# Kernel optimization log

Hardware: AMD Instinct MI355X
Metric: run time of the kernel (lower is better)

## Reference

```python
import jax, jax.numpy as jnp
import numpy as np

N_NODES = 100000
N_GRAPHS = 64
NEG_SLOPE = 0.1


def lrelu(x):
    return jnp.where(x > 0, x, NEG_SLOPE * x)


def gcn_layer(x, W, b, src, dst, deg_inv_sqrt):
    # PyG GCNConv: x' = D^-1/2 (A + I) D^-1/2 (x W) + b
    h = x @ W  # [N, out]
    norm = (deg_inv_sqrt[src] * deg_inv_sqrt[dst])[:, None]  # [E, 1]
    agg = jax.ops.segment_sum(h[src] * norm, dst, num_segments=N_NODES)
    agg = agg + h * (deg_inv_sqrt ** 2)[:, None]  # self-loop contribution
    return agg + b


def setup_inputs() -> dict:
    key = jax.random.key(0)
    ks = jax.random.split(key, 12)
    E = 1600000
    x = jax.random.normal(ks[0], (N_NODES, 128), dtype=jnp.float32)
    edge_index = jax.random.randint(ks[1], (2, E), 0, N_NODES, dtype=jnp.int32)
    batch = jnp.sort(jax.random.randint(ks[2], (N_NODES,), 0, N_GRAPHS, dtype=jnp.int32))

    def glorot(k, shape):
        fan_in, fan_out = shape
        s = jnp.sqrt(6.0 / (fan_in + fan_out))
        return jax.random.uniform(k, shape, jnp.float32, -s, s)

    return {
        "x": x,
        "edge_index": edge_index,
        "batch": batch,
        "W1": glorot(ks[3], (128, 32)),
        "b1": jnp.zeros((32,), jnp.float32),
        "W2": glorot(ks[4], (32, 64)),
        "b2": jnp.zeros((64,), jnp.float32),
        "Wl1": glorot(ks[5], (64, 128)),
        "bl1": jnp.zeros((128,), jnp.float32),
        "Wl2": glorot(ks[6], (128, 64)),
        "bl2": jnp.zeros((64,), jnp.float32),
        "Wl3": glorot(ks[7], (64, 1)),
        "bl3": jnp.zeros((1,), jnp.float32),
    }


def reference(x, edge_index, batch, W1, b1, W2, b2, Wl1, bl1, Wl2, bl2, Wl3, bl3):
    src, dst = edge_index[0], edge_index[1]
    # degree with self-loops (symmetric norm, all edge weights = 1)
    deg = jax.ops.segment_sum(jnp.ones_like(src, dtype=x.dtype), dst, num_segments=N_NODES) + 1.0
    deg_inv_sqrt = jax.lax.rsqrt(deg)

    h = lrelu(gcn_layer(x, W1, b1, src, dst, deg_inv_sqrt))
    h = gcn_layer(h, W2, b2, src, dst, deg_inv_sqrt)
    g = jax.ops.segment_max(h, batch, num_segments=N_GRAPHS)  # global max pool [G, 64]
    g = lrelu(g @ Wl1 + bl1)
    g = lrelu(g @ Wl2 + bl2)
    return g @ Wl3 + bl3  # [G, 1]
```

## Files before the change

kernel.cpp:

```cpp
#include <hip/hip_runtime.h>
#include <hip/hip_fp16.h>
#include <math.h>

#define N_NODES 100000
#define N_EDGES 1600000
#define N_GRAPHS 64
#define NB 391
#define CAP 5504

__device__ __forceinline__ unsigned f2o(float f) {
    unsigned u = __float_as_uint(f);
    return (u & 0x80000000u) ? ~u : (u | 0x80000000u);
}
__device__ __forceinline__ float o2f(unsigned u) {
    return (u & 0x80000000u) ? __uint_as_float(u & 0x7fffffffu) : __uint_as_float(~u);
}

__device__ __forceinline__ float4 cvt8(float2 raw) {
    __half2 h0 = ((const __half2*)&raw)[0];
    __half2 h1 = ((const __half2*)&raw)[1];
    float2 f0 = __half22float2(h0);
    float2 f1 = __half22float2(h1);
    return make_float4(f0.x, f0.y, f1.x, f1.y);
}
__device__ __forceinline__ float4 loadh8(const __half* p) {
    return cvt8(*(const float2*)p);
}
__device__ __forceinline__ void storeh8(__half* p, float4 v) {
    __half2 o0 = __floats2half2_rn(v.x, v.y);
    __half2 o1 = __floats2half2_rn(v.z, v.w);
    float2 ow;
    ((__half2*)&ow)[0] = o0;
    ((__half2*)&ow)[1] = o1;
    *(float2*)p = ow;
}

typedef _Float16 h2r __attribute__((ext_vector_type(2)));
typedef _Float16 h4  __attribute__((ext_vector_type(4)));
union HB { float4 f4; h2r h[4]; };
union H4 { float2 f2; h4 h; };

__global__ __launch_bounds__(256) void bucket_kernel(const int* __restrict__ src, const int* __restrict__ dst,
                                                     int* __restrict__ bucketCursor, unsigned* __restrict__ ebuf) {
    __shared__ int hist[NB];
    __shared__ int lbase[NB];
    __shared__ int lcur[NB];
    __shared__ int gbase[NB];
    __shared__ unsigned lbuf[3200];
    __shared__ unsigned short bkt[3200];
    int tid = threadIdx.x;
    for (int b = tid; b < NB; b += 256) hist[b] = 0;
    __syncthreads();
    int e0 = blockIdx.x * 3200;
    for (int i = tid; i < 3200; i += 256) {
        int d = dst[e0 + i];
        atomicAdd(&hist[d >> 8], 1);
    }
    __syncthreads();
    if (tid < 64) {
        int carry = 0;
        #pragma unroll
        for (int c = 0; c < 7; c++) {
            int idx = c * 64 + tid;
            int v = (idx < NB) ? hist[idx] : 0;
            int inc = v;
            #pragma unroll
            for (int o = 1; o < 64; o <<= 1) {
                int t = __shfl_up(inc, o, 64);
                if (tid >= o) inc += t;
            }
            if (idx < NB) lbase[idx] = carry + inc - v;
            carry += __shfl(inc, 63, 64);
        }
    }
    __syncthreads();
    for (int b = tid; b < NB; b += 256) {
        int h = hist[b];
        gbase[b] = h ? atomicAdd(&bucketCursor[b], h) : 0;
        lcur[b] = lbase[b];
    }
    __syncthreads();
    for (int i = tid; i < 3200; i += 256) {
        int d = dst[e0 + i];
        int s = src[e0 + i];
        int bu = d >> 8;
        int lp = atomicAdd(&lcur[bu], 1);
        lbuf[lp] = ((unsigned)(d & 255) << 24) | (unsigned)s;
        bkt[lp] = (unsigned short)bu;
    }
    __syncthreads();
    for (int i = tid; i < 3200; i += 256) {
        int bu = bkt[i];
        int off = gbase[bu] + (i - lbase[bu]);
        if (off < CAP)
            ebuf[(size_t)bu * CAP + off] = lbuf[i];
    }
}

__global__ __launch_bounds__(256) void csr_kernel(const unsigned* __restrict__ ebuf,
                                                  const int* __restrict__ bucketCursor,
                                                  int* __restrict__ colb, int* __restrict__ rowptr,
                                                  int* __restrict__ cnt, float* __restrict__ dis) {
    __shared__ unsigned stage1[CAP];
    __shared__ unsigned stage2[CAP];
    __shared__ int c256[256], row256[256], cur256[256];
    int b = blockIdx.x;
    int tid = threadIdx.x;
    int M = bucketCursor[b];
    if (M > CAP) M = CAP;
    c256[tid] = 0;
    __syncthreads();
    const unsigned* eb = ebuf + (size_t)b * CAP;
    for (int i = tid; i < M; i += 256) {
        unsigned v = eb[i];
        stage1[i] = v;
        atomicAdd(&c256[v >> 24], 1);
    }
    __syncthreads();
    if (tid < 64) {
        int c0 = c256[tid * 4], c1 = c256[tid * 4 + 1], c2 = c256[tid * 4 + 2], c3 = c256[tid * 4 + 3];
        int s = c0 + c1 + c2 + c3;
        int inc = s;
        #pragma unroll
        for (int o = 1; o < 64; o <<= 1) {
            int v = __shfl_up(inc, o, 64);
            if (tid >= o) inc += v;
        }
        int ex = inc - s;
        row256[tid * 4] = ex;
        row256[tid * 4 + 1] = ex + c0;
        row256[tid * 4 + 2] = ex + c0 + c1;
        row256[tid * 4 + 3] = ex + c0 + c1 + c2;
    }
    __syncthreads();
    cur256[tid] = row256[tid];
    int node = (b << 8) + tid;
    if (node < N_NODES) {
        int c = c256[tid];
        cnt[node] = c;
        dis[node] = rsqrtf((float)(c + 1));
        rowptr[node] = b * CAP + row256[tid];
    }
    __syncthreads();
    for (int i = tid; i < M; i += 256) {
        unsigned p = stage1[i];
        int slot = atomicAdd(&cur256[p >> 24], 1);
        stage2[slot] = p & 0xFFFFFFu;
    }
    __syncthreads();
    for (int i = tid; i < M; i += 256) colb[b * CAP + i] = (int)stage2[i];
}

__global__ __launch_bounds__(256) void gemm1_kernel(const float* __restrict__ x, const float* __restrict__ W1,
                                                    const float* __restrict__ dis, __half* __restrict__ hs1h) {
    __shared__ __half xsh[128][136];
    __shared__ __half wth[32][136];
    int tid = threadIdx.x;
    int r0 = blockIdx.x * 128;
    for (int idx = tid; idx < 128 * 32; idx += 256) {
        int k = idx >> 5, j = idx & 31;
        wth[j][k] = __float2half_rn(W1[idx]);
    }
    for (int idx = tid; idx < 128 * 32; idx += 256) {
        int r = idx >> 5, c4 = idx & 31;
        int gr = r0 + r;
        float4 v = (gr < N_NODES) ? ((const float4*)x)[(size_t)gr * 32 + c4] : make_float4(0.f, 0.f, 0.f, 0.f);
        __half* p = &xsh[r][c4 * 4];
        *(__half2*)p       = __floats2half2_rn(v.x, v.y);
        *(__half2*)(p + 2) = __floats2half2_rn(v.z, v.w);
    }
    __syncthreads();
    int jg = tid & 7;
    int rg = tid >> 3;
    float acc[4][4];
    #pragma unroll
    for (int i = 0; i < 4; i++)
        #pragma unroll
        for (int j = 0; j < 4; j++) acc[i][j] = 0.f;
    for (int kc = 0; kc < 128; kc += 8) {
        HB xr[4], wr[4];
        #pragma unroll
        for (int ri = 0; ri < 4; ri++) xr[ri].f4 = *(const float4*)&xsh[rg + 32 * ri][kc];
        #pragma unroll
        for (int jj = 0; jj < 4; jj++) wr[jj].f4 = *(const float4*)&wth[jg * 4 + jj][kc];
        #pragma unroll
        for (int ri = 0; ri < 4; ri++) {
            #pragma unroll
            for (int jj = 0; jj < 4; jj++) {
                #pragma unroll
                for (int t = 0; t < 4; t++) {
#if defined(__has_builtin) && __has_builtin(__builtin_amdgcn_fdot2)
                    acc[ri][jj] = __builtin_amdgcn_fdot2(xr[ri].h[t], wr[jj].h[t], acc[ri][jj], false);
#else
                    acc[ri][jj] += (float)xr[ri].h[t][0] * (float)wr[jj].h[t][0]
                                 + (float)xr[ri].h[t][1] * (float)wr[jj].h[t][1];
#endif
                }
            }
        }
    }
    #pragma unroll
    for (int ri = 0; ri < 4; ri++) {
        int gr = r0 + rg + 32 * ri;
        if (gr < N_NODES) {
            float dr = dis[gr];
            float2 ow;
            ((__half2*)&ow)[0] = __floats2half2_rn(dr * acc[ri][0], dr * acc[ri][1]);
            ((__half2*)&ow)[1] = __floats2half2_rn(dr * acc[ri][2], dr * acc[ri][3]);
            *(float2*)&hs1h[(size_t)gr * 32 + jg * 4] = ow;
        }
    }
}

__global__ __launch_bounds__(256) void agg1_kernel(const __half* __restrict__ hs1h, const int* __restrict__ colb,
                                                   const int* __restrict__ rowptr, const int* __restrict__ cnt,
                                                   const float* __restrict__ dis, const float* __restrict__ b1,
                                                   __half* __restrict__ t1h) {
    int tid = threadIdx.x;
    int wid = tid >> 6;
    int lane = tid & 63;
    int half = lane >> 5;
    int es = (lane >> 3) & 3;
    int q = lane & 7;
    int w = blockIdx.x * 4 + wid;
    int r0 = w * 4;

    H4 z; z.f2 = make_float2(0.f, 0.f);
    int r = r0 + half;
    int st = rowptr[r];
    int n = cnt[r];
    H4 pS = z, p0 = z, p1 = z, p2 = z, p3 = z, p4 = z, p5 = z;
    if (es == 0) pS.f2 = *(const float2*)(hs1h + (size_t)r * 32 + q * 4);
    {
        int e0 = es, e1 = 4 + es, e2 = 8 + es, e3 = 12 + es, e4 = 16 + es, e5 = 20 + es;
        if (e0 < n) p0.f2 = *(const float2*)(hs1h + (size_t)colb[st + e0] * 32 + q * 4);
        if (e1 < n) p1.f2 = *(const float2*)(hs1h + (size_t)colb[st + e1] * 32 + q * 4);
        if (e2 < n) p2.f2 = *(const float2*)(hs1h + (size_t)colb[st + e2] * 32 + q * 4);
        if (e3 < n) p3.f2 = *(const float2*)(hs1h + (size_t)colb[st + e3] * 32 + q * 4);
        if (e4 < n) p4.f2 = *(const float2*)(hs1h + (size_t)colb[st + e4] * 32 + q * 4);
        if (e5 < n) p5.f2 = *(const float2*)(hs1h + (size_t)colb[st + e5] * 32 + q * 4);
    }
    #pragma unroll
    for (int i = 0; i < 2; i++) {
        int rA = r;
        int stA = st, nA = n;
        H4 rS = pS, v0 = p0, v1 = p1, v2 = p2, v3 = p3, v4 = p4, v5 = p5;
        pS = z; p0 = z; p1 = z; p2 = z; p3 = z; p4 = z; p5 = z;
        if (i == 0) {
            r = r0 + 2 + half;
            st = rowptr[r];
            n = cnt[r];
            if (es == 0) pS.f2 = *(const float2*)(hs1h + (size_t)r * 32 + q * 4);
            int e0 = es, e1 = 4 + es, e2 = 8 + es, e3 = 12 + es, e4 = 16 + es, e5 = 20 + es;
            if (e0 < n) p0.f2 = *(const float2*)(hs1h + (size_t)colb[st + e0] * 32 + q * 4);
            if (e1 < n) p1.f2 = *(const float2*)(hs1h + (size_t)colb[st + e1] * 32 + q * 4);
            if (e2 < n) p2.f2 = *(const float2*)(hs1h + (size_t)colb[st + e2] * 32 + q * 4);
            if (e3 < n) p3.f2 = *(const float2*)(hs1h + (size_t)colb[st + e3] * 32 + q * 4);
            if (e4 < n) p4.f2 = *(const float2*)(hs1h + (size_t)colb[st + e4] * 32 + q * 4);
            if (e5 < n) p5.f2 = *(const float2*)(hs1h + (size_t)colb[st + e5] * 32 + q * 4);
        }
        h4 sh = (rS.h + (v0.h + v1.h)) + ((v2.h + v3.h) + (v4.h + v5.h));
        float4 a = make_float4((float)sh.x, (float)sh.y, (float)sh.z, (float)sh.w);
        for (int k = 24; k < nA; k += 8) {
            int e0 = k + es, e1 = k + 4 + es;
            if (e0 < nA) {
                float4 v = loadh8(hs1h + (size_t)colb[stA + e0] * 32 + q * 4);
                a.x += v.x; a.y += v.y; a.z += v.z; a.w += v.w;
            }
            if (e1 < nA) {
                float4 v = loadh8(hs1h + (size_t)colb[stA + e1] * 32 + q * 4);
                a.x += v.x; a.y += v.y; a.z += v.z; a.w += v.w;
            }
        }
        #pragma unroll
        for (int m = 8; m <= 16; m <<= 1) {
            a.x += __shfl_xor(a.x, m, 64);
            a.y += __shfl_xor(a.y, m, 64);
            a.z += __shfl_xor(a.z, m, 64);
            a.w += __shfl_xor(a.w, m, 64);
        }
        if (es == 0) {
            float4 bv = *(const float4*)&b1[q * 4];
            float dr = dis[rA];
            float4 v;
            v.x = dr * a.x + bv.x; v.y = dr * a.y + bv.y; v.z = dr * a.z + bv.z; v.w = dr * a.w + bv.w;
            v.x = v.x > 0.f ? v.x : 0.1f * v.x;
            v.y = v.y > 0.f ? v.y : 0.1f * v.y;
            v.z = v.z > 0.f ? v.z : 0.1f * v.z;
            v.w = v.w > 0.f ? v.w : 0.1f * v.w;
            v.x *= dr; v.y *= dr; v.z *= dr; v.w *= dr;
            storeh8(t1h + (size_t)rA * 32 + q * 4, v);
        }
    }
}

__global__ __launch_bounds__(1024) void agg2gemm_kernel(const __half* __restrict__ t1h, const int* __restrict__ colb,
                                                        const int* __restrict__ rowptr, const int* __restrict__ cnt,
                                                        const float* __restrict__ dis,
                                                        const float* __restrict__ W2, const float* __restrict__ b2,
                                                        const int* __restrict__ batch, unsigned* __restrict__ gbufu) {
    __shared__ float as1[64][32];
    __shared__ float w2s[32][64];
    __shared__ float red[16][64];
    int tid = threadIdx.x;
    int r0 = blockIdx.x * 64;
    for (int idx = tid; idx < 32 * 64; idx += 1024) w2s[idx >> 6][idx & 63] = W2[idx];

    int wid = tid >> 6;
    int lane = tid & 63;
    int half = lane >> 5;
    int es = (lane >> 3) & 3;
    int q = lane & 7;
    int base = r0 + wid * 4;

    H4 z; z.f2 = make_float2(0.f, 0.f);
    int r = base + half;
    bool vld = r < N_NODES;
    int st = vld ? rowptr[r] : 0;
    int n  = vld ? cnt[r] : 0;
    H4 pS = z, p0 = z, p1 = z, p2 = z, p3 = z, p4 = z, p5 = z;
    if (vld && es == 0) pS.f2 = *(const float2*)(t1h + (size_t)r * 32 + q * 4);
    {
        int e0 = es, e1 = 4 + es, e2 = 8 + es, e3 = 12 + es, e4 = 16 + es, e5 = 20 + es;
        if (e0 < n) p0.f2 = *(const float2*)(t1h + (size_t)colb[st + e0] * 32 + q * 4);
        if (e1 < n) p1.f2 = *(const float2*)(t1h + (size_t)colb[st + e1] * 32 + q * 4);
        if (e2 < n) p2.f2 = *(const float2*)(t1h + (size_t)colb[st + e2] * 32 + q * 4);
        if (e3 < n) p3.f2 = *(const float2*)(t1h + (size_t)colb[st + e3] * 32 + q * 4);
        if (e4 < n) p4.f2 = *(const float2*)(t1h + (size_t)colb[st + e4] * 32 + q * 4);
        if (e5 < n) p5.f2 = *(const float2*)(t1h + (size_t)colb[st + e5] * 32 + q * 4);
    }
    #pragma unroll
    for (int i = 0; i < 2; i++) {
        int rA = i * 2;
        int rAg = base + rA + half;
        bool vA = rAg < N_NODES;
        int stA = st, nA = n;
        H4 rS = pS, v0 = p0, v1 = p1, v2 = p2, v3 = p3, v4 = p4, v5 = p5;
        pS = z; p0 = z; p1 = z; p2 = z; p3 = z; p4 = z; p5 = z;
        if (i == 0) {
            r = base + 2 + half;
            vld = r < N_NODES;
            st = vld ? rowptr[r] : 0;
            n  = vld ? cnt[r] : 0;
            if (vld && es == 0) pS.f2 = *(const float2*)(t1h + (size_t)r * 32 + q * 4);
            int e0 = es, e1 = 4 + es, e2 = 8 + es, e3 = 12 + es, e4 = 16 + es, e5 = 20 + es;
            if (e0 < n) p0.f2 = *(const float2*)(t1h + (size_t)colb[st + e0] * 32 + q * 4);
            if (e1 < n) p1.f2 = *(const float2*)(t1h + (size_t)colb[st + e1] * 32 + q * 4);
            if (e2 < n) p2.f2 = *(const float2*)(t1h + (size_t)colb[st + e2] * 32 + q * 4);
            if (e3 < n) p3.f2 = *(const float2*)(t1h + (size_t)colb[st + e3] * 32 + q * 4);
            if (e4 < n) p4.f2 = *(const float2*)(t1h + (size_t)colb[st + e4] * 32 + q * 4);
            if (e5 < n) p5.f2 = *(const float2*)(t1h + (size_t)colb[st + e5] * 32 + q * 4);
        }
        h4 sh = (rS.h + (v0.h + v1.h)) + ((v2.h + v3.h) + (v4.h + v5.h));
        float4 a = make_float4((float)sh.x, (float)sh.y, (float)sh.z, (float)sh.w);
        for (int k = 24; k < nA; k += 8) {
            int e0 = k + es, e1 = k + 4 + es;
            if (e0 < nA) {
                float4 v = loadh8(t1h + (size_t)colb[stA + e0] * 32 + q * 4);
                a.x += v.x; a.y += v.y; a.z += v.z; a.w += v.w;
            }
            if (e1 < nA) {
                float4 v = loadh8(t1h + (size_t)colb[stA + e1] * 32 + q * 4);
                a.x += v.x; a.y += v.y; a.z += v.z; a.w += v.w;
            }
        }
        #pragma unroll
        for (int m = 8; m <= 16; m <<= 1) {
            a.x += __shfl_xor(a.x, m, 64);
            a.y += __shfl_xor(a.y, m, 64);
            a.z += __shfl_xor(a.z, m, 64);
            a.w += __shfl_xor(a.w, m, 64);
        }
        if (es == 0 && vA) {
            float dr = dis[rAg];
            float4 o = make_float4(dr * a.x, dr * a.y, dr * a.z, dr * a.w);
            *(float4*)&as1[wid * 4 + rA + half][q * 4] = o;
        }
    }
    __syncthreads();

    int j = tid & 63;
    int rq = tid >> 6;
    float w2c[32];
    #pragma unroll
    for (int k = 0; k < 32; k++) w2c[k] = w2s[k][j];
    float bj = b2[j];
    int rend = (r0 + 64 <= N_NODES) ? 64 : (N_NODES - r0);
    int gfirst = batch[r0];
    int glast = batch[r0 + rend - 1];
    bool uni = (gfirst == glast);
    float runmax = -INFINITY;
    #pragma unroll
    for (int i = 0; i < 4; i++) {
        int rl = rq + i * 16;
        if (rl >= rend) break;
        float acc = bj;
        #pragma unroll
        for (int kc = 0; kc < 32; kc += 4) {
            float4 av = *(const float4*)&as1[rl][kc];
            acc += av.x * w2c[kc] + av.y * w2c[kc + 1] + av.z * w2c[kc + 2] + av.w * w2c[kc + 3];
        }
        if (uni) runmax = fmaxf(runmax, acc);
        else atomicMax(&gbufu[batch[r0 + rl] * 64 + j], f2o(acc));
    }
    if (uni) {
        red[rq][j] = runmax;
        __syncthreads();
        if (tid < 64) {
            float m = -INFINITY;
            #pragma unroll
            for (int k = 0; k < 16; k++) m = fmaxf(m, red[k][tid]);
            atomicMax(&gbufu[gfirst * 64 + tid], f2o(m));
        }
    }
}

__global__ __launch_bounds__(256) void mlp_kernel(const unsigned* __restrict__ gbufu,
                                                  const float* __restrict__ Wl1, const float* __restrict__ bl1,
                                                  const float* __restrict__ Wl2, const float* __restrict__ bl2,
                                                  const float* __restrict__ Wl3, const float* __restrict__ bl3,
                                                  float* __restrict__ out) {
    __shared__ float A[64][64];
    __shared__ float B[64][128];
    int tid = threadIdx.x;
    for (int idx = tid; idx < 64 * 64; idx += 256) A[idx >> 6][idx & 63] = o2f(gbufu[idx]);
    __syncthreads();
    {
        int j = tid & 127;
        int rg = tid >> 7;
        float wc[64];
        #pragma unroll
        for (int k = 0; k < 64; k++) wc[k] = Wl1[k * 128 + j];
        float bj = bl1[j];
        for (int r = rg; r < 64; r += 2) {
            float acc = bj;
            #pragma unroll
            for (int kc = 0; kc < 64; kc += 4) {
                float4 av = *(const float4*)&A[r][kc];
                acc += av.x * wc[kc] + av.y * wc[kc + 1] + av.z * wc[kc + 2] + av.w * wc[kc + 3];
            }
            B[r][j] = acc > 0.f ? acc : 0.1f * acc;
        }
    }
    __syncthreads();
    {
        int j = tid & 63;
        int rg = tid >> 6;
        float wc[128];
        #pragma unroll
        for (int k = 0; k < 128; k++) wc[k] = Wl2[k * 64 + j];
        float bj = bl2[j];
        for (int r = rg; r < 64; r += 4) {
            float acc = bj;
            #pragma unroll
            for (int kc = 0; kc < 128; kc += 4) {
                float4 bv = *(const float4*)&B[r][kc];
                acc += bv.x * wc[kc] + bv.y * wc[kc + 1] + bv.z * wc[kc + 2] + bv.w * wc[kc + 3];
            }
            A[r][j] = acc > 0.f ? acc : 0.1f * acc;
        }
    }
    __syncthreads();
    if (tid < 64) {
        int r = tid;
        float acc = bl3[0];
        #pragma unroll
        for (int k = 0; k < 64; k++) acc += A[r][k] * Wl3[k];
        out[r] = acc;
    }
}

extern "C" void kernel_launch(void* const* d_in, const int* in_sizes, int n_in,
                              void* d_out, int out_size, void* d_ws, size_t ws_size,
                              hipStream_t stream) {
    (void)in_sizes; (void)n_in; (void)out_size; (void)ws_size;
    const float* x    = (const float*)d_in[0];
    const int*   edge = (const int*)d_in[1];
    const int*   batch= (const int*)d_in[2];
    const float* W1   = (const float*)d_in[3];
    const float* b1   = (const float*)d_in[4];
    const float* W2   = (const float*)d_in[5];
    const float* b2   = (const float*)d_in[6];
    const float* Wl1  = (const float*)d_in[7];
    const float* bl1  = (const float*)d_in[8];
    const float* Wl2  = (const float*)d_in[9];
    const float* bl2  = (const float*)d_in[10];
    const float* Wl3  = (const float*)d_in[11];
    const float* bl3  = (const float*)d_in[12];
    const int* srcp = edge;
    const int* dstp = edge + N_EDGES;

    char* ws = (char*)d_ws;
    int*      bucketCursor = (int*)ws;
    unsigned* gbufu        = (unsigned*)(bucketCursor + NB);
    size_t zeroed = (size_t)(NB + N_GRAPHS * 64) * 4;
    size_t off = (zeroed + 255) & ~(size_t)255;
    auto alloc = [&](size_t bytes) { char* p = ws + off; off = (off + bytes + 255) & ~(size_t)255; return p; };
    float*    dis    = (float*)alloc((size_t)N_NODES * 4);
    int*      cnt    = (int*)alloc((size_t)N_NODES * 4);
    int*      rowptr = (int*)alloc((size_t)N_NODES * 4);
    unsigned* ebuf   = (unsigned*)alloc((size_t)NB * CAP * 4);
    int*      colb   = (int*)alloc((size_t)NB * CAP * 4);
    __half*   hs1h   = (__half*)alloc((size_t)N_NODES * 32 * 2);
    __half*   t1h    = (__half*)alloc((size_t)N_NODES * 32 * 2);

    hipMemsetAsync(ws, 0, zeroed, stream);

    bucket_kernel  <<<500, 256, 0, stream>>>(srcp, dstp, bucketCursor, ebuf);
    csr_kernel     <<<NB, 256, 0, stream>>>(ebuf, bucketCursor, colb, rowptr, cnt, dis);
    gemm1_kernel   <<<(N_NODES + 127) / 128, 256, 0, stream>>>(x, W1, dis, hs1h);
    agg1_kernel    <<<6250, 256, 0, stream>>>(hs1h, colb, rowptr, cnt, dis, b1, t1h);
    agg2gemm_kernel<<<(N_NODES + 63) / 64, 1024, 0, stream>>>(t1h, colb, rowptr, cnt, dis, W2, b2, batch, gbufu);
    mlp_kernel     <<<1, 256, 0, stream>>>(gbufu, Wl1, bl1, Wl2, bl2, Wl3, bl3, (float*)d_out);
}
```

Before: 262.4 us.

## Replace CSR build with bucketed edge lists and LDS atomic aggregation

The full CSR construction (per-bucket sort into colb, rowptr, cnt) is dropped; the CSR kernel now only counts degrees to produce dis. Both aggregation kernels instead read the raw bucketed edge buffer. Each block takes one quarter of a 256-node bucket, compacts its edges into LDS with a ballot, gathers the source features and accumulates them with shared-memory float atomics. This removes the second sort pass and the colb/rowptr traffic. In exchange every block rescans the whole bucket, pays for LDS atomic contention, and silently drops edges beyond ELMAX=2048 per quarter.

```diff
diff --git a/kernel.cpp b/kernel.cpp
--- a/kernel.cpp
+++ b/kernel.cpp
@@ -7,6 +7,7 @@
 #define N_GRAPHS 64
 #define NB 391
 #define CAP 5504
+#define ELMAX 2048
 
 __device__ __forceinline__ unsigned f2o(float f) {
     unsigned u = __float_as_uint(f);
@@ -97,13 +98,10 @@
     }
 }
 
-__global__ __launch_bounds__(256) void csr_kernel(const unsigned* __restrict__ ebuf,
-                                                  const int* __restrict__ bucketCursor,
-                                                  int* __restrict__ colb, int* __restrict__ rowptr,
-                                                  int* __restrict__ cnt, float* __restrict__ dis) {
-    __shared__ unsigned stage1[CAP];
-    __shared__ unsigned stage2[CAP];
-    __shared__ int c256[256], row256[256], cur256[256];
+__global__ __launch_bounds__(256) void csrlite_kernel(const unsigned* __restrict__ ebuf,
+                                                      const int* __restrict__ bucketCursor,
+                                                      float* __restrict__ dis) {
+    __shared__ int c256[256];
     int b = blockIdx.x;
     int tid = threadIdx.x;
     int M = bucketCursor[b];
@@ -111,44 +109,10 @@
     c256[tid] = 0;
     __syncthreads();
     const unsigned* eb = ebuf + (size_t)b * CAP;
-    for (int i = tid; i < M; i += 256) {
-        unsigned v = eb[i];
-        stage1[i] = v;
-        atomicAdd(&c256[v >> 24], 1);
-    }
-    __syncthreads();
-    if (tid < 64) {
-        int c0 = c256[tid * 4], c1 = c256[tid * 4 + 1], c2 = c256[tid * 4 + 2], c3 = c256[tid * 4 + 3];
-        int s = c0 + c1 + c2 + c3;
-        int inc = s;
-        #pragma unroll
-        for (int o = 1; o < 64; o <<= 1) {
-            int v = __shfl_up(inc, o, 64);
-            if (tid >= o) inc += v;
-        }
-        int ex = inc - s;
-        row256[tid * 4] = ex;
-        row256[tid * 4 + 1] = ex + c0;
-        row256[tid * 4 + 2] = ex + c0 + c1;
-        row256[tid * 4 + 3] = ex + c0 + c1 + c2;
-    }
-    __syncthreads();
-    cur256[tid] = row256[tid];
+    for (int i = tid; i < M; i += 256) atomicAdd(&c256[eb[i] >> 24], 1);
+    __syncthreads();
     int node = (b << 8) + tid;
-    if (node < N_NODES) {
-        int c = c256[tid];
-        cnt[node] = c;
-        dis[node] = rsqrtf((float)(c + 1));
-        rowptr[node] = b * CAP + row256[tid];
-    }
-    __syncthreads();
-    for (int i = tid; i < M; i += 256) {
-        unsigned p = stage1[i];
-        int slot = atomicAdd(&cur256[p >> 24], 1);
-        stage2[slot] = p & 0xFFFFFFu;
-    }
-    __syncthreads();
-    for (int i = tid; i < M; i += 256) colb[b * CAP + i] = (int)stage2[i];
+    if (node < N_NODES) dis[node] = rsqrtf((float)(c256[tid] + 1));
 }
 
 __global__ __launch_bounds__(256) void gemm1_kernel(const float* __restrict__ x, const float* __restrict__ W1,
@@ -212,169 +176,194 @@
     }
 }
 
-__global__ __launch_bounds__(256) void agg1_kernel(const __half* __restrict__ hs1h, const int* __restrict__ colb,
-                                                   const int* __restrict__ rowptr, const int* __restrict__ cnt,
-                                                   const float* __restrict__ dis, const float* __restrict__ b1,
-                                                   __half* __restrict__ t1h) {
+#define ACCP 36
+
+__global__ __launch_bounds__(512) void agg1e_kernel(const __half* __restrict__ hs1h,
+                                                    const unsigned* __restrict__ ebuf,
+                                                    const int* __restrict__ bucketCursor,
+                                                    const float* __restrict__ dis, const float* __restrict__ b1,
+                                                    __half* __restrict__ t1h) {
+    __shared__ float acc[64][ACCP];
+    __shared__ unsigned elist[ELMAX];
+    __shared__ int ecnt;
     int tid = threadIdx.x;
+    int b = blockIdx.x >> 2;
+    int qt = blockIdx.x & 3;
+    int nb = (b << 8) + (qt << 6);
+    for (int i = tid; i < 64 * ACCP; i += 512) ((float*)acc)[i] = 0.f;
+    if (tid == 0) ecnt = 0;
+    __syncthreads();
+
+    int M = bucketCursor[b];
+    if (M > CAP) M = CAP;
+    const unsigned* eb = ebuf + (size_t)b * CAP;
+    int lane = tid & 63;
+    for (int i0 = 0; i0 < M; i0 += 512) {
+        int i = i0 + tid;
+        unsigned w = 0;
+        bool keep = false;
+        if (i < M) {
+            w = eb[i];
+            keep = ((w >> 30) == (unsigned)qt);
+        }
+        unsigned long long m = __ballot(keep);
+        int cnt = __popcll(m);
+        int base = 0;
+        if (lane == 0 && cnt) base = atomicAdd(&ecnt, cnt);
+        base = __shfl(base, 0, 64);
+        if (keep) {
+            int slot = base + __popcll(m & ((1ull << lane) - 1ull));
+            if (slot < ELMAX) elist[slot] = w;
+        }
+    }
+    __syncthreads();
+    int E = ecnt;
+    if (E > ELMAX) E = ELMAX;
+
     int wid = tid >> 6;
-    int lane = tid & 63;
-    int half = lane >> 5;
-    int es = (lane >> 3) & 3;
+    int e = lane >> 3;
     int q = lane & 7;
-    int w = blockIdx.x * 4 + wid;
-    int r0 = w * 4;
-
     H4 z; z.f2 = make_float2(0.f, 0.f);
-    int r = r0 + half;
-    int st = rowptr[r];
-    int n = cnt[r];
-    H4 pS = z, p0 = z, p1 = z, p2 = z, p3 = z, p4 = z, p5 = z;
-    if (es == 0) pS.f2 = *(const float2*)(hs1h + (size_t)r * 32 + q * 4);
+    H4 pv = z; int pdl = -1;
     {
-        int e0 = es, e1 = 4 + es, e2 = 8 + es, e3 = 12 + es, e4 = 16 + es, e5 = 20 + es;
-        if (e0 < n) p0.f2 = *(const float2*)(hs1h + (size_t)colb[st + e0] * 32 + q * 4);
-        if (e1 < n) p1.f2 = *(const float2*)(hs1h + (size_t)colb[st + e1] * 32 + q * 4);
-        if (e2 < n) p2.f2 = *(const float2*)(hs1h + (size_t)colb[st + e2] * 32 + q * 4);
-        if (e3 < n) p3.f2 = *(const float2*)(hs1h + (size_t)colb[st + e3] * 32 + q * 4);
-        if (e4 < n) p4.f2 = *(const float2*)(hs1h + (size_t)colb[st + e4] * 32 + q * 4);
-        if (e5 < n) p5.f2 = *(const float2*)(hs1h + (size_t)colb[st + e5] * 32 + q * 4);
-    }
-    #pragma unroll
-    for (int i = 0; i < 2; i++) {
-        int rA = r;
-        int stA = st, nA = n;
-        H4 rS = pS, v0 = p0, v1 = p1, v2 = p2, v3 = p3, v4 = p4, v5 = p5;
-        pS = z; p0 = z; p1 = z; p2 = z; p3 = z; p4 = z; p5 = z;
-        if (i == 0) {
-            r = r0 + 2 + half;
-            st = rowptr[r];
-            n = cnt[r];
-            if (es == 0) pS.f2 = *(const float2*)(hs1h + (size_t)r * 32 + q * 4);
-            int e0 = es, e1 = 4 + es, e2 = 8 + es, e3 = 12 + es, e4 = 16 + es, e5 = 20 + es;
-            if (e0 < n) p0.f2 = *(const float2*)(hs1h + (size_t)colb[st + e0] * 32 + q * 4);
-            if (e1 < n) p1.f2 = *(const float2*)(hs1h + (size_t)colb[st + e1] * 32 + q * 4);
-            if (e2 < n) p2.f2 = *(const float2*)(hs1h + (size_t)colb[st + e2] * 32 + q * 4);
-            if (e3 < n) p3.f2 = *(const float2*)(hs1h + (size_t)colb[st + e3] * 32 + q * 4);
-            if (e4 < n) p4.f2 = *(const float2*)(hs1h + (size_t)colb[st + e4] * 32 + q * 4);
-            if (e5 < n) p5.f2 = *(const float2*)(hs1h + (size_t)colb[st + e5] * 32 + q * 4);
-        }
-        h4 sh = (rS.h + (v0.h + v1.h)) + ((v2.h + v3.h) + (v4.h + v5.h));
-        float4 a = make_float4((float)sh.x, (float)sh.y, (float)sh.z, (float)sh.w);
-        for (int k = 24; k < nA; k += 8) {
-            int e0 = k + es, e1 = k + 4 + es;
-            if (e0 < nA) {
-                float4 v = loadh8(hs1h + (size_t)colb[stA + e0] * 32 + q * 4);
-                a.x += v.x; a.y += v.y; a.z += v.z; a.w += v.w;
-            }
-            if (e1 < nA) {
-                float4 v = loadh8(hs1h + (size_t)colb[stA + e1] * 32 + q * 4);
-                a.x += v.x; a.y += v.y; a.z += v.z; a.w += v.w;
-            }
-        }
-        #pragma unroll
-        for (int m = 8; m <= 16; m <<= 1) {
-            a.x += __shfl_xor(a.x, m, 64);
-            a.y += __shfl_xor(a.y, m, 64);
-            a.z += __shfl_xor(a.z, m, 64);
-            a.w += __shfl_xor(a.w, m, 64);
-        }
-        if (es == 0) {
-            float4 bv = *(const float4*)&b1[q * 4];
-            float dr = dis[rA];
-            float4 v;
-            v.x = dr * a.x + bv.x; v.y = dr * a.y + bv.y; v.z = dr * a.z + bv.z; v.w = dr * a.w + bv.w;
-            v.x = v.x > 0.f ? v.x : 0.1f * v.x;
-            v.y = v.y > 0.f ? v.y : 0.1f * v.y;
-            v.z = v.z > 0.f ? v.z : 0.1f * v.z;
-            v.w = v.w > 0.f ? v.w : 0.1f * v.w;
-            v.x *= dr; v.y *= dr; v.z *= dr; v.w *= dr;
-            storeh8(t1h + (size_t)rA * 32 + q * 4, v);
-        }
-    }
-}
-
-__global__ __launch_bounds__(1024) void agg2gemm_kernel(const __half* __restrict__ t1h, const int* __restrict__ colb,
-                                                        const int* __restrict__ rowptr, const int* __restrict__ cnt,
-                                                        const float* __restrict__ dis,
-                                                        const float* __restrict__ W2, const float* __restrict__ b2,
-                                                        const int* __restrict__ batch, unsigned* __restrict__ gbufu) {
-    __shared__ float as1[64][32];
+        int gi = wid * 8 + e;
+        if (gi < E) {
+            unsigned w = elist[gi];
+            pdl = (int)((w >> 24) & 63u);
+            pv.f2 = *(const float2*)(hs1h + (size_t)(w & 0xFFFFFFu) * 32 + q * 4);
+        }
+    }
+    for (int bi = wid * 8; bi < E; bi += 64) {
+        H4 cv = pv; int cdl = pdl;
+        pv = z; pdl = -1;
+        int gi = bi + 64 + e;
+        if (gi < E) {
+            unsigned w = elist[gi];
+            pdl = (int)((w >> 24) & 63u);
+            pv.f2 = *(const float2*)(hs1h + (size_t)(w & 0xFFFFFFu) * 32 + q * 4);
+        }
+        if (cdl >= 0) {
+            float4 f = cvt8(cv.f2);
+            atomicAdd(&acc[cdl][q * 4 + 0], f.x);
+            atomicAdd(&acc[cdl][q * 4 + 1], f.y);
+            atomicAdd(&acc[cdl][q * 4 + 2], f.z);
+            atomicAdd(&acc[cdl][q * 4 + 3], f.w);
+        }
+    }
+    __syncthreads();
+
+    int row = tid >> 3, qc = tid & 7;
+    int node = nb + row;
+    if (node < N_NODES) {
+        float dr = dis[node];
+        float4 s = loadh8(hs1h + (size_t)node * 32 + qc * 4);
+        float4 a = *(const float4*)&acc[row][qc * 4];
+        float4 bv = *(const float4*)&b1[qc * 4];
+        float4 v;
+        v.x = dr * (a.x + s.x) + bv.x;
+        v.y = dr * (a.y + s.y) + bv.y;
+        v.z = dr * (a.z + s.z) + bv.z;
+        v.w = dr * (a.w + s.w) + bv.w;
+        v.x = v.x > 0.f ? v.x : 0.1f * v.x;
+        v.y = v.y > 0.f ? v.y : 0.1f * v.y;
+        v.z = v.z > 0.f ? v.z : 0.1f * v.z;
+        v.w = v.w > 0.f ? v.w : 0.1f * v.w;
+        v.x *= dr; v.y *= dr; v.z *= dr; v.w *= dr;
+        storeh8(t1h + (size_t)node * 32 + qc * 4, v);
+    }
+}
+
+__global__ __launch_bounds__(512) void agg2e_kernel(const __half* __restrict__ t1h,
+                                                    const unsigned* __restrict__ ebuf,
+                                                    const int* __restrict__ bucketCursor,
+                                                    const float* __restrict__ dis,
+                                                    const float* __restrict__ W2, const float* __restrict__ b2,
+                                                    const int* __restrict__ batch, unsigned* __restrict__ gbufu) {
+    __shared__ float acc[64][ACCP];
+    __shared__ unsigned elist[ELMAX];
     __shared__ float w2s[32][64];
-    __shared__ float red[16][64];
+    __shared__ float red[8][64];
+    __shared__ int ecnt;
     int tid = threadIdx.x;
     int r0 = blockIdx.x * 64;
-    for (int idx = tid; idx < 32 * 64; idx += 1024) w2s[idx >> 6][idx & 63] = W2[idx];
+    if (r0 >= N_NODES) return;
+    int b = blockIdx.x >> 2;
+    int qt = blockIdx.x & 3;
+    for (int i = tid; i < 64 * ACCP; i += 512) ((float*)acc)[i] = 0.f;
+    for (int idx = tid; idx < 32 * 64; idx += 512) w2s[idx >> 6][idx & 63] = W2[idx];
+    if (tid == 0) ecnt = 0;
+    __syncthreads();
+
+    int M = bucketCursor[b];
+    if (M > CAP) M = CAP;
+    const unsigned* eb = ebuf + (size_t)b * CAP;
+    int lane = tid & 63;
+    for (int i0 = 0; i0 < M; i0 += 512) {
+        int i = i0 + tid;
+        unsigned w = 0;
+        bool keep = false;
+        if (i < M) {
+            w = eb[i];
+            keep = ((w >> 30) == (unsigned)qt);
+        }
+        unsigned long long m = __ballot(keep);
+        int cnt = __popcll(m);
+        int base = 0;
+        if (lane == 0 && cnt) base = atomicAdd(&ecnt, cnt);
+        base = __shfl(base, 0, 64);
+        if (keep) {
+            int slot = base + __popcll(m & ((1ull << lane) - 1ull));
+            if (slot < ELMAX) elist[slot] = w;
+        }
+    }
+    __syncthreads();
+    int E = ecnt;
+    if (E > ELMAX) E = ELMAX;
 
     int wid = tid >> 6;
-    int lane = tid & 63;
-    int half = lane >> 5;
-    int es = (lane >> 3) & 3;
+    int e = lane >> 3;
     int q = lane & 7;
-    int base = r0 + wid * 4;
-
     H4 z; z.f2 = make_float2(0.f, 0.f);
-    int r = base + half;
-    bool vld = r < N_NODES;
-    int st = vld ? rowptr[r] : 0;
-    int n  = vld ? cnt[r] : 0;
-    H4 pS = z, p0 = z, p1 = z, p2 = z, p3 = z, p4 = z, p5 = z;
-    if (vld && es == 0) pS.f2 = *(const float2*)(t1h + (size_t)r * 32 + q * 4);
+    H4 pv = z; int pdl = -1;
     {
-        int e0 = es, e1 = 4 + es, e2 = 8 + es, e3 = 12 + es, e4 = 16 + es, e5 = 20 + es;
-        if (e0 < n) p0.f2 = *(const float2*)(t1h + (size_t)colb[st + e0] * 32 + q * 4);
-        if (e1 < n) p1.f2 = *(const float2*)(t1h + (size_t)colb[st + e1] * 32 + q * 4);
-        if (e2 < n) p2.f2 = *(const float2*)(t1h + (size_t)colb[st + e2] * 32 + q * 4);
-        if (e3 < n) p3.f2 = *(const float2*)(t1h + (size_t)colb[st + e3] * 32 + q * 4);
-        if (e4 < n) p4.f2 = *(const float2*)(t1h + (size_t)colb[st + e4] * 32 + q * 4);
-        if (e5 < n) p5.f2 = *(const float2*)(t1h + (size_t)colb[st + e5] * 32 + q * 4);
-    }
-    #pragma unroll
-    for (int i = 0; i < 2; i++) {
-        int rA = i * 2;
-        int rAg = base + rA + half;
-        bool vA = rAg < N_NODES;
-        int stA = st, nA = n;
-        H4 rS = pS, v0 = p0, v1 = p1, v2 = p2, v3 = p3, v4 = p4, v5 = p5;
-        pS = z; p0 = z; p1 = z; p2 = z; p3 = z; p4 = z; p5 = z;
-        if (i == 0) {
-            r = base + 2 + half;
-            vld = r < N_NODES;
-            st = vld ? rowptr[r] : 0;
-            n  = vld ? cnt[r] : 0;
-            if (vld && es == 0) pS.f2 = *(const float2*)(t1h + (size_t)r * 32 + q * 4);
-            int e0 = es, e1 = 4 + es, e2 = 8 + es, e3 = 12 + es, e4 = 16 + es, e5 = 20 + es;
-            if (e0 < n) p0.f2 = *(const float2*)(t1h + (size_t)colb[st + e0] * 32 + q * 4);
-            if (e1 < n) p1.f2 = *(const float2*)(t1h + (size_t)colb[st + e1] * 32 + q * 4);
-            if (e2 < n) p2.f2 = *(const float2*)(t1h + (size_t)colb[st + e2] * 32 + q * 4);
-            if (e3 < n) p3.f2 = *(const float2*)(t1h + (size_t)colb[st + e3] * 32 + q * 4);
-            if (e4 < n) p4.f2 = *(const float2*)(t1h + (size_t)colb[st + e4] * 32 + q * 4);
-            if (e5 < n) p5.f2 = *(const float2*)(t1h + (size_t)colb[st + e5] * 32 + q * 4);
-        }
-        h4 sh = (rS.h + (v0.h + v1.h)) + ((v2.h + v3.h) + (v4.h + v5.h));
-        float4 a = make_float4((float)sh.x, (float)sh.y, (float)sh.z, (float)sh.w);
-        for (int k = 24; k < nA; k += 8) {
-            int e0 = k + es, e1 = k + 4 + es;
-            if (e0 < nA) {
-                float4 v = loadh8(t1h + (size_t)colb[stA + e0] * 32 + q * 4);
-                a.x += v.x; a.y += v.y; a.z += v.z; a.w += v.w;
-            }
-            if (e1 < nA) {
-                float4 v = loadh8(t1h + (size_t)colb[stA + e1] * 32 + q * 4);
-                a.x += v.x; a.y += v.y; a.z += v.z; a.w += v.w;
-            }
-        }
-        #pragma unroll
-        for (int m = 8; m <= 16; m <<= 1) {
-            a.x += __shfl_xor(a.x, m, 64);
-            a.y += __shfl_xor(a.y, m, 64);
-            a.z += __shfl_xor(a.z, m, 64);
-            a.w += __shfl_xor(a.w, m, 64);
-        }
-        if (es == 0 && vA) {
-            float dr = dis[rAg];
-            float4 o = make_float4(dr * a.x, dr * a.y, dr * a.z, dr * a.w);
-            *(float4*)&as1[wid * 4 + rA + half][q * 4] = o;
+        int gi = wid * 8 + e;
+        if (gi < E) {
+            unsigned w = elist[gi];
+            pdl = (int)((w >> 24) & 63u);
+            pv.f2 = *(const float2*)(t1h + (size_t)(w & 0xFFFFFFu) * 32 + q * 4);
+        }
+    }
+    for (int bi = wid * 8; bi < E; bi += 64) {
+        H4 cv = pv; int cdl = pdl;
+        pv = z; pdl = -1;
+        int gi = bi + 64 + e;
+        if (gi < E) {
+            unsigned w = elist[gi];
+            pdl = (int)((w >> 24) & 63u);
+            pv.f2 = *(const float2*)(t1h + (size_t)(w & 0xFFFFFFu) * 32 + q * 4);
+        }
+        if (cdl >= 0) {
+            float4 f = cvt8(cv.f2);
+            atomicAdd(&acc[cdl][q * 4 + 0], f.x);
+            atomicAdd(&acc[cdl][q * 4 + 1], f.y);
+            atomicAdd(&acc[cdl][q * 4 + 2], f.z);
+            atomicAdd(&acc[cdl][q * 4 + 3], f.w);
+        }
+    }
+    __syncthreads();
+
+    {
+        int row = tid >> 3, qc = tid & 7;
+        int node = r0 + row;
+        if (node < N_NODES) {
+            float dr = dis[node];
+            float4 s = loadh8(t1h + (size_t)node * 32 + qc * 4);
+            float4 a = *(const float4*)&acc[row][qc * 4];
+            a.x = dr * (a.x + s.x);
+            a.y = dr * (a.y + s.y);
+            a.z = dr * (a.z + s.z);
+            a.w = dr * (a.w + s.w);
+            *(float4*)&acc[row][qc * 4] = a;
         }
     }
     __syncthreads();
@@ -391,17 +380,17 @@
     bool uni = (gfirst == glast);
     float runmax = -INFINITY;
     #pragma unroll
-    for (int i = 0; i < 4; i++) {
-        int rl = rq + i * 16;
+    for (int i = 0; i < 8; i++) {
+        int rl = rq + i * 8;
         if (rl >= rend) break;
-        float acc = bj;
+        float acc2 = bj;
         #pragma unroll
         for (int kc = 0; kc < 32; kc += 4) {
-            float4 av = *(const float4*)&as1[rl][kc];
-            acc += av.x * w2c[kc] + av.y * w2c[kc + 1] + av.z * w2c[kc + 2] + av.w * w2c[kc + 3];
-        }
-        if (uni) runmax = fmaxf(runmax, acc);
-        else atomicMax(&gbufu[batch[r0 + rl] * 64 + j], f2o(acc));
+            float4 av = *(const float4*)&acc[rl][kc];
+            acc2 += av.x * w2c[kc] + av.y * w2c[kc + 1] + av.z * w2c[kc + 2] + av.w * w2c[kc + 3];
+        }
+        if (uni) runmax = fmaxf(runmax, acc2);
+        else atomicMax(&gbufu[batch[r0 + rl] * 64 + j], f2o(acc2));
     }
     if (uni) {
         red[rq][j] = runmax;
@@ -409,7 +398,7 @@
         if (tid < 64) {
             float m = -INFINITY;
             #pragma unroll
-            for (int k = 0; k < 16; k++) m = fmaxf(m, red[k][tid]);
+            for (int k = 0; k < 8; k++) m = fmaxf(m, red[k][tid]);
             atomicMax(&gbufu[gfirst * 64 + tid], f2o(m));
         }
     }
@@ -497,19 +486,16 @@
     size_t off = (zeroed + 255) & ~(size_t)255;
     auto alloc = [&](size_t bytes) { char* p = ws + off; off = (off + bytes + 255) & ~(size_t)255; return p; };
     float*    dis    = (float*)alloc((size_t)N_NODES * 4);
-    int*      cnt    = (int*)alloc((size_t)N_NODES * 4);
-    int*      rowptr = (int*)alloc((size_t)N_NODES * 4);
     unsigned* ebuf   = (unsigned*)alloc((size_t)NB * CAP * 4);
-    int*      colb   = (int*)alloc((size_t)NB * CAP * 4);
     __half*   hs1h   = (__half*)alloc((size_t)N_NODES * 32 * 2);
     __half*   t1h    = (__half*)alloc((size_t)N_NODES * 32 * 2);
 
     hipMemsetAsync(ws, 0, zeroed, stream);
 
-    bucket_kernel  <<<500, 256, 0, stream>>>(srcp, dstp, bucketCursor, ebuf);
-    csr_kernel     <<<NB, 256, 0, stream>>>(ebuf, bucketCursor, colb, rowptr, cnt, dis);
-    gemm1_kernel   <<<(N_NODES + 127) / 128, 256, 0, stream>>>(x, W1, dis, hs1h);
-    agg1_kernel    <<<6250, 256, 0, stream>>>(hs1h, colb, rowptr, cnt, dis, b1, t1h);
-    agg2gemm_kernel<<<(N_NODES + 63) / 64, 1024, 0, stream>>>(t1h, colb, rowptr, cnt, dis, W2, b2, batch, gbufu);
-    mlp_kernel     <<<1, 256, 0, stream>>>(gbufu, Wl1, bl1, Wl2, bl2, Wl3, bl3, (float*)d_out);
-}
+    bucket_kernel <<<500, 256, 0, stream>>>(srcp, dstp, bucketCursor, ebuf);
+    csrlite_kernel<<<NB, 256, 0, stream>>>(ebuf, bucketCursor, dis);
+    gemm1_kernel  <<<(N_NODES + 127) / 128, 256, 0, stream>>>(x, W1, dis, hs1h);
+    agg1e_kernel  <<<NB * 4, 512, 0, stream>>>(hs1h, ebuf, bucketCursor, dis, b1, t1h);
+    agg2e_kernel  <<<NB * 4, 512, 0, stream>>>(t1h, ebuf, bucketCursor, dis, W2, b2, batch, gbufu);
+    mlp_kernel    <<<1, 256, 0, stream>>>(gbufu, Wl1, bl1, Wl2, bl2, Wl3, bl3, (float*)d_out);
+}
```

Result: slower. 807.2 us (+207.7%).
